# Performance work log

Hardware: AMD Instinct MI355X
Metric: run time of the kernel (lower is better)

Reference implementation:

```python
import jax, jax.numpy as jnp
import numpy as np

EMB_DIM = 500
GAMMA = 12.0
NUM_ENTITIES = 14541
NUM_RELATIONS = 474
PI = 3.141592653589793
RANGE = (GAMMA + 2.0) / EMB_DIM  # embedding_range from the RotatE config


def setup_inputs() -> dict:
    key = jax.random.key(0)
    k1, k2, k3, k4 = jax.random.split(key, 4)
    B = 16
    all_h = jax.random.randint(k1, (B,), 0, NUM_ENTITIES, dtype=jnp.int64)
    all_r = jax.random.randint(k2, (B,), 0, NUM_RELATIONS, dtype=jnp.int64)
    # entity embeddings hold [re | im] halves -> 2*EMB_DIM columns
    eemb = jax.random.normal(k3, (NUM_ENTITIES, 2 * EMB_DIM), dtype=jnp.float32)
    remb = jax.random.normal(k4, (NUM_RELATIONS, EMB_DIM), dtype=jnp.float32)
    return {"all_h": all_h, "all_r": all_r, "eemb": eemb, "remb": remb}


def reference(all_h, all_r, eemb, remb):
    # gather head / relation embeddings
    h = eemb[all_h]                      # [B, 2D]
    re_h, im_h = jnp.split(h, 2, axis=-1)  # [B, D] each
    # project: phase -> unit complex number
    phase = remb[all_r] / (RANGE / PI)   # [B, D]
    re_r, im_r = jnp.cos(phase), jnp.sin(phase)
    # complex rotation of the head
    re_rot = re_h * re_r - im_h * im_r   # [B, D]
    im_rot = re_h * im_r + im_h * re_r   # [B, D]
    # diff against every entity (tail), complex modulus, L1 over dim
    re_t, im_t = jnp.split(eemb, 2, axis=-1)          # [E, D]
    re_diff = re_rot[:, None, :] - re_t[None, :, :]   # [B, E, D]
    im_diff = im_rot[:, None, :] - im_t[None, :, :]   # [B, E, D]
    dist = jnp.sqrt(re_diff ** 2 + im_diff ** 2).sum(axis=-1)  # [B, E]
    return GAMMA - dist
```

## Files before the change

kernel.cpp:

```cpp
#include <hip/hip_runtime.h>
#include <hip/hip_fp16.h>
#include <math.h>

#define EMB_DIM 500
#define TWO_D 1000
#define D4 125
#define ROW_F4 250
#define NUM_ENTITIES 14541
#define B_SIZE 16
#define GAMMA_F 12.0f
#define PHASE_SCALE 112.19973762820692f
#define ROT_HALFS (B_SIZE * D4 * 8)

__global__ __launch_bounds__(256) void rot_precompute(
    const int* __restrict__ all_h, const int* __restrict__ all_r,
    const float* __restrict__ eemb, const float* __restrict__ remb,
    __half* __restrict__ rot)
{
    int i = blockIdx.x * 256 + threadIdx.x;
    if (i >= B_SIZE * EMB_DIM) return;
    int b = i / EMB_DIM;
    int d = i - b * EMB_DIM;
    int h = all_h[b];
    int r = all_r[b];
    float re_h = eemb[h * TWO_D + d];
    float im_h = eemb[h * TWO_D + EMB_DIM + d];
    float ph = remb[r * EMB_DIM + d] * PHASE_SCALE;
    float s, c;
    sincosf(ph, &s, &c);
    int base = ((b * D4 + (d >> 2)) << 3) + (d & 3);
    rot[base]     = __float2half(re_h * c - im_h * s);
    rot[base + 4] = __float2half(re_h * s + im_h * c);
}

__global__ __launch_bounds__(256, 4) void rotate_score(
    const float* __restrict__ eemb,
    const __half* __restrict__ rot,
    const int* __restrict__ all_h, const int* __restrict__ all_r,
    const float* __restrict__ remb,
    float* __restrict__ out)
{
    __shared__ __half lrot[ROT_HALFS];

    const int tid = threadIdx.x;

    if (rot != nullptr) {
        const float4* src = (const float4*)rot;
        float4* dst = (float4*)lrot;
        for (int i = tid; i < ROT_HALFS / 8; i += 256) dst[i] = src[i];
    } else {
        for (int i = tid; i < B_SIZE * EMB_DIM; i += 256) {
            int b = i / EMB_DIM;
            int d = i - b * EMB_DIM;
            int h = all_h[b];
            int r = all_r[b];
            float re_h = eemb[h * TWO_D + d];
            float im_h = eemb[h * TWO_D + EMB_DIM + d];
            float ph = remb[r * EMB_DIM + d] * PHASE_SCALE;
            float s, c;
            sincosf(ph, &s, &c);
            int base = ((b * D4 + (d >> 2)) << 3) + (d & 3);
            lrot[base]     = __float2half(re_h * c - im_h * s);
            lrot[base + 4] = __float2half(re_h * s + im_h * c);
        }
    }
    __syncthreads();

    const int lane = tid & 63;
    const int wave = tid >> 6;
    const int e0 = blockIdx.x * 16 + wave * 4;

    int e[4];
#pragma unroll
    for (int k = 0; k < 4; ++k) {
        int ek = e0 + k;
        e[k] = (ek < NUM_ENTITIES) ? ek : (NUM_ENTITIES - 1);
    }

    float v[64];
#pragma unroll
    for (int i = 0; i < 64; ++i) v[i] = 0.0f;

    const float4* lrot4 = (const float4*)lrot;
    const float4* ee4 = (const float4*)eemb;

#pragma unroll
    for (int it = 0; it < 2; ++it) {
        const int d4 = it * 64 + lane;
        if (d4 < D4) {
            float4 tre[4], tim[4];
#pragma unroll
            for (int k = 0; k < 4; ++k) {
                int rb = e[k] * ROW_F4;
                tre[k] = ee4[rb + d4];
                tim[k] = ee4[rb + D4 + d4];
            }
#pragma unroll
            for (int b = 0; b < 16; ++b) {
                float4 rv = lrot4[b * D4 + d4];
                __half2 p0 = __builtin_bit_cast(__half2, rv.x);
                __half2 p1 = __builtin_bit_cast(__half2, rv.y);
                __half2 p2 = __builtin_bit_cast(__half2, rv.z);
                __half2 p3 = __builtin_bit_cast(__half2, rv.w);
                float rre0 = __low2float(p0), rre1 = __high2float(p0);
                float rre2 = __low2float(p1), rre3 = __high2float(p1);
                float rim0 = __low2float(p2), rim1 = __high2float(p2);
                float rim2 = __low2float(p3), rim3 = __high2float(p3);
#pragma unroll
                for (int k = 0; k < 4; ++k) {
                    float dre, dim;
                    dre = rre0 - tre[k].x; dim = rim0 - tim[k].x;
                    v[k * 16 + b] += __builtin_amdgcn_sqrtf(dre * dre + dim * dim);
                    dre = rre1 - tre[k].y; dim = rim1 - tim[k].y;
                    v[k * 16 + b] += __builtin_amdgcn_sqrtf(dre * dre + dim * dim);
                    dre = rre2 - tre[k].z; dim = rim2 - tim[k].z;
                    v[k * 16 + b] += __builtin_amdgcn_sqrtf(dre * dre + dim * dim);
                    dre = rre3 - tre[k].w; dim = rim3 - tim[k].w;
                    v[k * 16 + b] += __builtin_amdgcn_sqrtf(dre * dre + dim * dim);
                }
            }
        }
    }

#pragma unroll
    for (int m = 32; m >= 1; m >>= 1) {
        const bool hi = (lane & m) != 0;
#pragma unroll
        for (int i = 0; i < m; ++i) {
            float give = hi ? v[i] : v[m + i];
            float keep = hi ? v[m + i] : v[i];
            v[i] = keep + __shfl_xor(give, m, 64);
        }
    }

    const int kk = lane >> 4;
    const int bb = lane & 15;
    const int ee = e0 + kk;
    if (ee < NUM_ENTITIES) out[bb * NUM_ENTITIES + ee] = GAMMA_F - v[0];
}

extern "C" void kernel_launch(void* const* d_in, const int* in_sizes, int n_in,
                              void* d_out, int out_size, void* d_ws, size_t ws_size,
                              hipStream_t stream) {
    const int*   all_h = (const int*)d_in[0];
    const int*   all_r = (const int*)d_in[1];
    const float* eemb  = (const float*)d_in[2];
    const float* remb  = (const float*)d_in[3];
    float* out = (float*)d_out;

    __half* rot = nullptr;
    const size_t rot_bytes = (size_t)ROT_HALFS * sizeof(__half);
    if (ws_size >= rot_bytes) {
        rot = (__half*)d_ws;
        rot_precompute<<<(B_SIZE * EMB_DIM + 255) / 256, 256, 0, stream>>>(
            all_h, all_r, eemb, remb, rot);
    }

    int nblocks = (NUM_ENTITIES + 15) / 16;
    rotate_score<<<nblocks, 256, 0, stream>>>(eemb, rot, all_h, all_r, remb, out);
}
```

Before: 39.83 us.

## Split embedding dimension across blocks with partial sums and a combine kernel

The main scoring kernel now splits the 125 float4 columns into two halves handled by separate blocks. Each wave covers 2 entities instead of 4, and the rotated heads are loaded straight into registers from global memory instead of staged through LDS. Partial L1 sums go to a workspace buffer, and a third kernel adds the two halves and applies gamma. This raises parallelism, cuts register pressure and removes the LDS fill and barrier. In exchange it adds an extra launch, a round trip of partial sums through global memory, and idle lanes in the second half (61 of 64 valid).

Result: slower. 132.0 us (+231.4%).

```diff
diff --git a/kernel.cpp b/kernel.cpp
--- a/kernel.cpp
+++ b/kernel.cpp
@@ -11,6 +11,7 @@
 #define GAMMA_F 12.0f
 #define PHASE_SCALE 112.19973762820692f
 #define ROT_HALFS (B_SIZE * D4 * 8)
+#define NP (B_SIZE * NUM_ENTITIES)
 
 __global__ __launch_bounds__(256) void rot_precompute(
     const int* __restrict__ all_h, const int* __restrict__ all_r,
@@ -33,57 +34,151 @@
     rot[base + 4] = __float2half(re_h * s + im_h * c);
 }
 
-__global__ __launch_bounds__(256, 4) void rotate_score(
+__global__ __launch_bounds__(256) void rotate_partial(
     const float* __restrict__ eemb,
     const __half* __restrict__ rot,
+    float* __restrict__ partial)
+{
+    const int tid  = threadIdx.x;
+    const int lane = tid & 63;
+    const int wave = tid >> 6;
+    const int etile = blockIdx.x >> 1;
+    const int dh    = blockIdx.x & 1;
+    const int e0 = etile * 8 + wave * 2;
+
+    const int d4  = dh * 64 + lane;
+    const bool valid = (d4 < D4);
+    const int d4c = valid ? d4 : (D4 - 1);
+
+    const float4* rot4 = (const float4*)rot;
+    const float4* ee4  = (const float4*)eemb;
+
+    float4 rv[16];
+#pragma unroll
+    for (int b = 0; b < 16; ++b) rv[b] = rot4[b * D4 + d4c];
+
+    int e[2];
+#pragma unroll
+    for (int k = 0; k < 2; ++k) {
+        int ek = e0 + k;
+        e[k] = (ek < NUM_ENTITIES) ? ek : (NUM_ENTITIES - 1);
+    }
+
+    float4 tre[2], tim[2];
+#pragma unroll
+    for (int k = 0; k < 2; ++k) {
+        int rb = e[k] * ROW_F4;
+        tre[k] = ee4[rb + d4c];
+        tim[k] = ee4[rb + D4 + d4c];
+    }
+
+    float v[32];
+#pragma unroll
+    for (int i = 0; i < 32; ++i) v[i] = 0.0f;
+
+    if (valid) {
+#pragma unroll
+        for (int b = 0; b < 16; ++b) {
+            __half2 p0 = __builtin_bit_cast(__half2, rv[b].x);
+            __half2 p1 = __builtin_bit_cast(__half2, rv[b].y);
+            __half2 p2 = __builtin_bit_cast(__half2, rv[b].z);
+            __half2 p3 = __builtin_bit_cast(__half2, rv[b].w);
+            float rre0 = __low2float(p0), rre1 = __high2float(p0);
+            float rre2 = __low2float(p1), rre3 = __high2float(p1);
+            float rim0 = __low2float(p2), rim1 = __high2float(p2);
+            float rim2 = __low2float(p3), rim3 = __high2float(p3);
+#pragma unroll
+            for (int k = 0; k < 2; ++k) {
+                float dre, dim;
+                dre = rre0 - tre[k].x; dim = rim0 - tim[k].x;
+                v[k * 16 + b] += __builtin_amdgcn_sqrtf(dre * dre + dim * dim);
+                dre = rre1 - tre[k].y; dim = rim1 - tim[k].y;
+                v[k * 16 + b] += __builtin_amdgcn_sqrtf(dre * dre + dim * dim);
+                dre = rre2 - tre[k].z; dim = rim2 - tim[k].z;
+                v[k * 16 + b] += __builtin_amdgcn_sqrtf(dre * dre + dim * dim);
+                dre = rre3 - tre[k].w; dim = rim3 - tim[k].w;
+                v[k * 16 + b] += __builtin_amdgcn_sqrtf(dre * dre + dim * dim);
+            }
+        }
+    }
+
+#pragma unroll
+    for (int i = 0; i < 32; ++i) v[i] += __shfl_xor(v[i], 32, 64);
+#pragma unroll
+    for (int m = 16; m >= 1; m >>= 1) {
+        const bool hi = (lane & m) != 0;
+#pragma unroll
+        for (int i = 0; i < m; ++i) {
+            float give = hi ? v[i] : v[m + i];
+            float keep = hi ? v[m + i] : v[i];
+            v[i] = keep + __shfl_xor(give, m, 64);
+        }
+    }
+
+    if (lane < 32) {
+        const int kk = lane >> 4;
+        const int bb = lane & 15;
+        const int ee = e0 + kk;
+        if (ee < NUM_ENTITIES)
+            partial[dh * NP + bb * NUM_ENTITIES + ee] = v[0];
+    }
+}
+
+__global__ __launch_bounds__(256) void combine(
+    const float* __restrict__ partial, float* __restrict__ out)
+{
+    int i = blockIdx.x * 256 + threadIdx.x;
+    const int n4 = NP / 4;
+    if (i >= n4) return;
+    const float4* p0 = (const float4*)partial;
+    const float4* p1 = (const float4*)(partial + NP);
+    float4 a = p0[i], b = p1[i];
+    float4 r;
+    r.x = GAMMA_F - (a.x + b.x);
+    r.y = GAMMA_F - (a.y + b.y);
+    r.z = GAMMA_F - (a.z + b.z);
+    r.w = GAMMA_F - (a.w + b.w);
+    ((float4*)out)[i] = r;
+}
+
+__global__ __launch_bounds__(256) void rotate_score_fb(
+    const float* __restrict__ eemb,
     const int* __restrict__ all_h, const int* __restrict__ all_r,
     const float* __restrict__ remb,
     float* __restrict__ out)
 {
     __shared__ __half lrot[ROT_HALFS];
-
     const int tid = threadIdx.x;
-
-    if (rot != nullptr) {
-        const float4* src = (const float4*)rot;
-        float4* dst = (float4*)lrot;
-        for (int i = tid; i < ROT_HALFS / 8; i += 256) dst[i] = src[i];
-    } else {
-        for (int i = tid; i < B_SIZE * EMB_DIM; i += 256) {
-            int b = i / EMB_DIM;
-            int d = i - b * EMB_DIM;
-            int h = all_h[b];
-            int r = all_r[b];
-            float re_h = eemb[h * TWO_D + d];
-            float im_h = eemb[h * TWO_D + EMB_DIM + d];
-            float ph = remb[r * EMB_DIM + d] * PHASE_SCALE;
-            float s, c;
-            sincosf(ph, &s, &c);
-            int base = ((b * D4 + (d >> 2)) << 3) + (d & 3);
-            lrot[base]     = __float2half(re_h * c - im_h * s);
-            lrot[base + 4] = __float2half(re_h * s + im_h * c);
-        }
+    for (int i = tid; i < B_SIZE * EMB_DIM; i += 256) {
+        int b = i / EMB_DIM;
+        int d = i - b * EMB_DIM;
+        int h = all_h[b];
+        int r = all_r[b];
+        float re_h = eemb[h * TWO_D + d];
+        float im_h = eemb[h * TWO_D + EMB_DIM + d];
+        float ph = remb[r * EMB_DIM + d] * PHASE_SCALE;
+        float s, c;
+        sincosf(ph, &s, &c);
+        int base = ((b * D4 + (d >> 2)) << 3) + (d & 3);
+        lrot[base]     = __float2half(re_h * c - im_h * s);
+        lrot[base + 4] = __float2half(re_h * s + im_h * c);
     }
     __syncthreads();
 
     const int lane = tid & 63;
     const int wave = tid >> 6;
     const int e0 = blockIdx.x * 16 + wave * 4;
-
     int e[4];
 #pragma unroll
     for (int k = 0; k < 4; ++k) {
         int ek = e0 + k;
         e[k] = (ek < NUM_ENTITIES) ? ek : (NUM_ENTITIES - 1);
     }
-
     float v[64];
 #pragma unroll
     for (int i = 0; i < 64; ++i) v[i] = 0.0f;
-
     const float4* lrot4 = (const float4*)lrot;
     const float4* ee4 = (const float4*)eemb;
-
 #pragma unroll
     for (int it = 0; it < 2; ++it) {
         const int d4 = it * 64 + lane;
@@ -97,11 +192,11 @@
             }
 #pragma unroll
             for (int b = 0; b < 16; ++b) {
-                float4 rv = lrot4[b * D4 + d4];
-                __half2 p0 = __builtin_bit_cast(__half2, rv.x);
-                __half2 p1 = __builtin_bit_cast(__half2, rv.y);
-                __half2 p2 = __builtin_bit_cast(__half2, rv.z);
-                __half2 p3 = __builtin_bit_cast(__half2, rv.w);
+                float4 rvb = lrot4[b * D4 + d4];
+                __half2 p0 = __builtin_bit_cast(__half2, rvb.x);
+                __half2 p1 = __builtin_bit_cast(__half2, rvb.y);
+                __half2 p2 = __builtin_bit_cast(__half2, rvb.z);
+                __half2 p3 = __builtin_bit_cast(__half2, rvb.w);
                 float rre0 = __low2float(p0), rre1 = __high2float(p0);
                 float rre2 = __low2float(p1), rre3 = __high2float(p1);
                 float rim0 = __low2float(p2), rim1 = __high2float(p2);
@@ -121,7 +216,6 @@
             }
         }
     }
-
 #pragma unroll
     for (int m = 32; m >= 1; m >>= 1) {
         const bool hi = (lane & m) != 0;
@@ -132,7 +226,6 @@
             v[i] = keep + __shfl_xor(give, m, 64);
         }
     }
-
     const int kk = lane >> 4;
     const int bb = lane & 15;
     const int ee = e0 + kk;
@@ -148,14 +241,18 @@
     const float* remb  = (const float*)d_in[3];
     float* out = (float*)d_out;
 
-    __half* rot = nullptr;
-    const size_t rot_bytes = (size_t)ROT_HALFS * sizeof(__half);
-    if (ws_size >= rot_bytes) {
-        rot = (__half*)d_ws;
+    const size_t part_bytes = (size_t)2 * NP * sizeof(float);
+    const size_t rot_bytes  = (size_t)ROT_HALFS * sizeof(__half);
+    if (ws_size >= part_bytes + rot_bytes) {
+        float*  part = (float*)d_ws;
+        __half* rot  = (__half*)((char*)d_ws + part_bytes);
         rot_precompute<<<(B_SIZE * EMB_DIM + 255) / 256, 256, 0, stream>>>(
             all_h, all_r, eemb, remb, rot);
-    }
-
-    int nblocks = (NUM_ENTITIES + 15) / 16;
-    rotate_score<<<nblocks, 256, 0, stream>>>(eemb, rot, all_h, all_r, remb, out);
-}
+        int etiles = (NUM_ENTITIES + 7) / 8;
+        rotate_partial<<<etiles * 2, 256, 0, stream>>>(eemb, rot, part);
+        combine<<<(NP / 4 + 255) / 256, 256, 0, stream>>>(part, out);
+    } else {
+        int nblocks = (NUM_ENTITIES + 15) / 16;
+        rotate_score_fb<<<nblocks, 256, 0, stream>>>(eemb, all_h, all_r, remb, out);
+    }
+}
```

## Split batch across two blocks per entity tile to halve accumulator registers

Applied to the files above, without the earlier changes.

Each entity tile is now handled by two blocks, each covering 8 of the 16 batch rows, so per-thread accumulators drop from 64 to 32 and the shared rotation buffer is halved. This lowers register pressure and doubles the grid, which should raise occupancy and latency hiding. The cost is that every entity row is read from global memory twice (once per block) and the reduction gains an extra shuffle stage. The old 16-batch kernel is kept as a fallback for when no workspace is provided.

New measurement: 96.69 us. 2.43x slower.

```diff
diff --git a/kernel.cpp b/kernel.cpp
--- a/kernel.cpp
+++ b/kernel.cpp
@@ -11,6 +11,7 @@
 #define GAMMA_F 12.0f
 #define PHASE_SCALE 112.19973762820692f
 #define ROT_HALFS (B_SIZE * D4 * 8)
+#define BLK_HALFS (8 * D4 * 8)
 
 __global__ __launch_bounds__(256) void rot_precompute(
     const int* __restrict__ all_h, const int* __restrict__ all_r,
@@ -33,25 +34,27 @@
     rot[base + 4] = __float2half(re_h * s + im_h * c);
 }
 
-__global__ __launch_bounds__(256, 4) void rotate_score(
+__global__ __launch_bounds__(256) void rotate_score(
     const float* __restrict__ eemb,
     const __half* __restrict__ rot,
     const int* __restrict__ all_h, const int* __restrict__ all_r,
     const float* __restrict__ remb,
     float* __restrict__ out)
 {
-    __shared__ __half lrot[ROT_HALFS];
+    __shared__ __half lrot[BLK_HALFS];
 
     const int tid = threadIdx.x;
+    const int bg  = blockIdx.x & 1;
 
     if (rot != nullptr) {
-        const float4* src = (const float4*)rot;
+        const float4* src = (const float4*)rot + bg * (BLK_HALFS / 8);
         float4* dst = (float4*)lrot;
-        for (int i = tid; i < ROT_HALFS / 8; i += 256) dst[i] = src[i];
+        for (int i = tid; i < BLK_HALFS / 8; i += 256) dst[i] = src[i];
     } else {
-        for (int i = tid; i < B_SIZE * EMB_DIM; i += 256) {
-            int b = i / EMB_DIM;
-            int d = i - b * EMB_DIM;
+        for (int i = tid; i < 8 * EMB_DIM; i += 256) {
+            int b8 = i / EMB_DIM;
+            int d = i - b8 * EMB_DIM;
+            int b = bg * 8 + b8;
             int h = all_h[b];
             int r = all_r[b];
             float re_h = eemb[h * TWO_D + d];
@@ -59,7 +62,7 @@
             float ph = remb[r * EMB_DIM + d] * PHASE_SCALE;
             float s, c;
             sincosf(ph, &s, &c);
-            int base = ((b * D4 + (d >> 2)) << 3) + (d & 3);
+            int base = ((b8 * D4 + (d >> 2)) << 3) + (d & 3);
             lrot[base]     = __float2half(re_h * c - im_h * s);
             lrot[base + 4] = __float2half(re_h * s + im_h * c);
         }
@@ -68,7 +71,7 @@
 
     const int lane = tid & 63;
     const int wave = tid >> 6;
-    const int e0 = blockIdx.x * 16 + wave * 4;
+    const int e0 = (blockIdx.x >> 1) * 16 + wave * 4;
 
     int e[4];
 #pragma unroll
@@ -77,9 +80,9 @@
         e[k] = (ek < NUM_ENTITIES) ? ek : (NUM_ENTITIES - 1);
     }
 
-    float v[64];
-#pragma unroll
-    for (int i = 0; i < 64; ++i) v[i] = 0.0f;
+    float v[32];
+#pragma unroll
+    for (int i = 0; i < 32; ++i) v[i] = 0.0f;
 
     const float4* lrot4 = (const float4*)lrot;
     const float4* ee4 = (const float4*)eemb;
@@ -96,8 +99,8 @@
                 tim[k] = ee4[rb + D4 + d4];
             }
 #pragma unroll
-            for (int b = 0; b < 16; ++b) {
-                float4 rv = lrot4[b * D4 + d4];
+            for (int b8 = 0; b8 < 8; ++b8) {
+                float4 rv = lrot4[b8 * D4 + d4];
                 __half2 p0 = __builtin_bit_cast(__half2, rv.x);
                 __half2 p1 = __builtin_bit_cast(__half2, rv.y);
                 __half2 p2 = __builtin_bit_cast(__half2, rv.z);
@@ -110,20 +113,22 @@
                 for (int k = 0; k < 4; ++k) {
                     float dre, dim;
                     dre = rre0 - tre[k].x; dim = rim0 - tim[k].x;
-                    v[k * 16 + b] += __builtin_amdgcn_sqrtf(dre * dre + dim * dim);
+                    v[k * 8 + b8] += __builtin_amdgcn_sqrtf(dre * dre + dim * dim);
                     dre = rre1 - tre[k].y; dim = rim1 - tim[k].y;
-                    v[k * 16 + b] += __builtin_amdgcn_sqrtf(dre * dre + dim * dim);
+                    v[k * 8 + b8] += __builtin_amdgcn_sqrtf(dre * dre + dim * dim);
                     dre = rre2 - tre[k].z; dim = rim2 - tim[k].z;
-                    v[k * 16 + b] += __builtin_amdgcn_sqrtf(dre * dre + dim * dim);
+                    v[k * 8 + b8] += __builtin_amdgcn_sqrtf(dre * dre + dim * dim);
                     dre = rre3 - tre[k].w; dim = rim3 - tim[k].w;
-                    v[k * 16 + b] += __builtin_amdgcn_sqrtf(dre * dre + dim * dim);
+                    v[k * 8 + b8] += __builtin_amdgcn_sqrtf(dre * dre + dim * dim);
                 }
             }
         }
     }
 
 #pragma unroll
-    for (int m = 32; m >= 1; m >>= 1) {
+    for (int i = 0; i < 32; ++i) v[i] += __shfl_xor(v[i], 32, 64);
+#pragma unroll
+    for (int m = 16; m >= 1; m >>= 1) {
         const bool hi = (lane & m) != 0;
 #pragma unroll
         for (int i = 0; i < m; ++i) {
@@ -133,6 +138,99 @@
         }
     }
 
+    if (lane < 32) {
+        const int kk = lane >> 3;
+        const int bb = bg * 8 + (lane & 7);
+        const int ee = e0 + kk;
+        if (ee < NUM_ENTITIES) out[bb * NUM_ENTITIES + ee] = GAMMA_F - v[0];
+    }
+}
+
+__global__ __launch_bounds__(256) void rotate_score_fb(
+    const float* __restrict__ eemb,
+    const int* __restrict__ all_h, const int* __restrict__ all_r,
+    const float* __restrict__ remb,
+    float* __restrict__ out)
+{
+    __shared__ __half lrot[ROT_HALFS];
+    const int tid = threadIdx.x;
+    for (int i = tid; i < B_SIZE * EMB_DIM; i += 256) {
+        int b = i / EMB_DIM;
+        int d = i - b * EMB_DIM;
+        int h = all_h[b];
+        int r = all_r[b];
+        float re_h = eemb[h * TWO_D + d];
+        float im_h = eemb[h * TWO_D + EMB_DIM + d];
+        float ph = remb[r * EMB_DIM + d] * PHASE_SCALE;
+        float s, c;
+        sincosf(ph, &s, &c);
+        int base = ((b * D4 + (d >> 2)) << 3) + (d & 3);
+        lrot[base]     = __float2half(re_h * c - im_h * s);
+        lrot[base + 4] = __float2half(re_h * s + im_h * c);
+    }
+    __syncthreads();
+
+    const int lane = tid & 63;
+    const int wave = tid >> 6;
+    const int e0 = blockIdx.x * 16 + wave * 4;
+    int e[4];
+#pragma unroll
+    for (int k = 0; k < 4; ++k) {
+        int ek = e0 + k;
+        e[k] = (ek < NUM_ENTITIES) ? ek : (NUM_ENTITIES - 1);
+    }
+    float v[64];
+#pragma unroll
+    for (int i = 0; i < 64; ++i) v[i] = 0.0f;
+    const float4* lrot4 = (const float4*)lrot;
+    const float4* ee4 = (const float4*)eemb;
+#pragma unroll
+    for (int it = 0; it < 2; ++it) {
+        const int d4 = it * 64 + lane;
+        if (d4 < D4) {
+            float4 tre[4], tim[4];
+#pragma unroll
+            for (int k = 0; k < 4; ++k) {
+                int rb = e[k] * ROW_F4;
+                tre[k] = ee4[rb + d4];
+                tim[k] = ee4[rb + D4 + d4];
+            }
+#pragma unroll
+            for (int b = 0; b < 16; ++b) {
+                float4 rvb = lrot4[b * D4 + d4];
+                __half2 p0 = __builtin_bit_cast(__half2, rvb.x);
+                __half2 p1 = __builtin_bit_cast(__half2, rvb.y);
+                __half2 p2 = __builtin_bit_cast(__half2, rvb.z);
+                __half2 p3 = __builtin_bit_cast(__half2, rvb.w);
+                float rre0 = __low2float(p0), rre1 = __high2float(p0);
+                float rre2 = __low2float(p1), rre3 = __high2float(p1);
+                float rim0 = __low2float(p2), rim1 = __high2float(p2);
+                float rim2 = __low2float(p3), rim3 = __high2float(p3);
+#pragma unroll
+                for (int k = 0; k < 4; ++k) {
+                    float dre, dim;
+                    dre = rre0 - tre[k].x; dim = rim0 - tim[k].x;
+                    v[k * 16 + b] += __builtin_amdgcn_sqrtf(dre * dre + dim * dim);
+                    dre = rre1 - tre[k].y; dim = rim1 - tim[k].y;
+                    v[k * 16 + b] += __builtin_amdgcn_sqrtf(dre * dre + dim * dim);
+                    dre = rre2 - tre[k].z; dim = rim2 - tim[k].z;
+                    v[k * 16 + b] += __builtin_amdgcn_sqrtf(dre * dre + dim * dim);
+                    dre = rre3 - tre[k].w; dim = rim3 - tim[k].w;
+                    v[k * 16 + b] += __builtin_amdgcn_sqrtf(dre * dre + dim * dim);
+                }
+            }
+        }
+    }
+#pragma unroll
+    for (int m = 32; m >= 1; m >>= 1) {
+        const bool hi = (lane & m) != 0;
+#pragma unroll
+        for (int i = 0; i < m; ++i) {
+            float give = hi ? v[i] : v[m + i];
+            float keep = hi ? v[m + i] : v[i];
+            v[i] = keep + __shfl_xor(give, m, 64);
+        }
+    }
     const int kk = lane >> 4;
     const int bb = lane & 15;
     const int ee = e0 + kk;
@@ -148,14 +246,17 @@
     const float* remb  = (const float*)d_in[3];
     float* out = (float*)d_out;
 
-    __half* rot = nullptr;
     const size_t rot_bytes = (size_t)ROT_HALFS * sizeof(__half);
     if (ws_size >= rot_bytes) {
-        rot = (__half*)d_ws;
+        __half* rot = (__half*)d_ws;
         rot_precompute<<<(B_SIZE * EMB_DIM + 255) / 256, 256, 0, stream>>>(
             all_h, all_r, eemb, remb, rot);
-    }
-
-    int nblocks = (NUM_ENTITIES + 15) / 16;
-    rotate_score<<<nblocks, 256, 0, stream>>>(eemb, rot, all_h, all_r, remb, out);
-}
+        int etiles = (NUM_ENTITIES + 15) / 16;
+        rotate_score<<<etiles * 2, 256, 0, stream>>>(
+            eemb, rot, all_h, all_r, remb, out);
+    } else {
+        int nblocks = (NUM_ENTITIES + 15) / 16;
+        rotate_score_fb<<<nblocks, 256, 0, stream>>>(
+            eemb, all_h, all_r, remb, out);
+    }
+}
```
